# Kernel tuning notes

Measured on AMD Instinct MI355X. Metric: run time of the kernel, lower is better.

## Reference

```python
import jax, jax.numpy as jnp
import numpy as np
from jax import lax

KS = 3
N = KS * KS  # 9 sampling locations per output pixel


def conv2d(x, w, b, pad, dil=1):
    out = lax.conv_general_dilated(
        x, w, window_strides=(1, 1), padding=((pad, pad), (pad, pad)),
        rhs_dilation=(dil, dil), dimension_numbers=('NCHW', 'OIHW', 'NCHW'))
    return out + b[None, :, None, None]


def deform_conv(x, p_w, p_b, dw, db):
    # Pure deform-conv-v2 semantics: offsets from p_conv, bilinear gather on
    # zero-padded input, then 3x3 contraction over the 9 gathered samples.
    B, C, H, W = x.shape
    offset = conv2d(x, p_w, p_b, 1)                       # (B, 2N, H, W)
    xp = jnp.pad(x, ((0, 0), (0, 0), (1, 1), (1, 1)))     # zero pad by 1
    Hp, Wp = H + 2, W + 2
    rr = jnp.arange(-(KS // 2), KS // 2 + 1)
    pi, pj = jnp.meshgrid(rr, rr, indexing='ij')
    p_n = jnp.concatenate([pi.reshape(-1), pj.reshape(-1)]).astype(x.dtype)   # (2N,)
    gi, gj = jnp.meshgrid(jnp.arange(1, H + 1), jnp.arange(1, W + 1), indexing='ij')
    p0 = jnp.concatenate([jnp.broadcast_to(gi, (N, H, W)),
                          jnp.broadcast_to(gj, (N, H, W))], 0).astype(x.dtype)  # (2N,H,W)
    p = p0[None] + p_n[None, :, None, None] + offset      # (B, 2N, H, W)
    p = jnp.transpose(p, (0, 2, 3, 1))                    # (B, H, W, 2N)
    py, px = p[..., :N], p[..., N:]
    fy, fx = jnp.floor(py), jnp.floor(px)
    lt_y = jnp.clip(fy, 0, Hp - 1); lt_x = jnp.clip(fx, 0, Wp - 1)
    rb_y = jnp.clip(fy + 1, 0, Hp - 1); rb_x = jnp.clip(fx + 1, 0, Wp - 1)
    pyc = jnp.clip(py, 0, Hp - 1); pxc = jnp.clip(px, 0, Wp - 1)
    g_lt = (1 + (lt_y - pyc)) * (1 + (lt_x - pxc))
    g_rb = (1 - (rb_y - pyc)) * (1 - (rb_x - pxc))
    g_lb = (1 + (lt_y - pyc)) * (1 - (rb_x - pxc))
    g_rt = (1 - (rb_y - pyc)) * (1 + (lt_x - pxc))
    xf = xp.reshape(B, C, Hp * Wp)

    def gather(qy, qx):
        idx = (qy.astype(jnp.int32) * Wp + qx.astype(jnp.int32)).reshape(B, -1)
        g = jax.vmap(lambda xb, ib: jnp.take(xb, ib, axis=1))(xf, idx)
        return g.reshape(B, C, H, W, N)

    x_lt = gather(lt_y, lt_x); x_rb = gather(rb_y, rb_x)
    x_lb = gather(lt_y, rb_x); x_rt = gather(rb_y, lt_x)
    samples = (g_lt[:, None] * x_lt + g_rb[:, None] * x_rb
               + g_lb[:, None] * x_lb + g_rt[:, None] * x_rt)  # (B,C,H,W,N)
    out = jnp.einsum('bchwn,ocn->bohw', samples, dw.reshape(dw.shape[0], C, N))
    return out + db[None, :, None, None]


def reference(x, w1, b1, w2, b2, w3, b3, w4, b4, p_w, p_b, dw, db, cw, cb):
    branches = [(w1, b1, 1, 1.0), (w2, b2, 3, 3.0), (w3, b3, 5, 5.0), (w4, b4, 7, 7.0)]
    feats = [deform_conv(conv2d(x, w, b, d, d) * s, p_w, p_b, dw, db)
             for (w, b, d, s) in branches]
    combined = jnp.concatenate(feats, axis=1)             # (B, 4*Cout, H, W)
    return jax.nn.relu(conv2d(combined, cw, cb, 0))


def setup_inputs() -> dict:
    B, Cin, Cout, H, W = 4, 128, 64, 128, 128
    key = jax.random.key(0)
    ks = jax.random.split(key, 16)
    sc3 = 1.0 / np.sqrt(Cin * 9)      # fan-in scale for 3x3 convs
    sc1 = 1.0 / np.sqrt(4 * Cout)     # fan-in scale for 1x1 fuse conv
    scd = 1.0 / np.sqrt(Cout * 9)     # deform main conv
    inp = {'x': jax.random.normal(ks[0], (B, Cin, H, W), jnp.float32)}
    for i in range(4):
        inp[f'w{i+1}'] = jax.random.normal(ks[1 + i], (Cout, Cin, 3, 3), jnp.float32) * sc3
        inp[f'b{i+1}'] = jax.random.normal(ks[5 + i], (Cout,), jnp.float32) * 0.01
    inp['p_w'] = jax.random.normal(ks[9], (2 * N, Cout, 3, 3), jnp.float32) * 0.01
    inp['p_b'] = jax.random.normal(ks[10], (2 * N,), jnp.float32) * 0.01
    inp['dw'] = jax.random.normal(ks[11], (Cout, Cout, 3, 3), jnp.float32) * scd
    inp['db'] = jax.random.normal(ks[12], (Cout,), jnp.float32) * 0.01
    inp['cw'] = jax.random.normal(ks[13], (Cout, 4 * Cout, 1, 1), jnp.float32) * sc1
    inp['cb'] = jax.random.normal(ks[14], (Cout,), jnp.float32) * 0.01
    return inp
```

## Files before the change

kernel.cpp:

```cpp
#include <hip/hip_runtime.h>
#include <hip/hip_fp16.h>

#define H 128
#define W 128
#define CIN 128
#define COUT 64
#define HW (H*W)
#define XW 130
#define FSL (XW*XW*64)
#define XTD 144

typedef __half f16;
typedef __attribute__((ext_vector_type(8)))  _Float16 h16x8;
typedef __attribute__((ext_vector_type(16))) float f32x16;

__device__ __forceinline__ float b2f(f16 v){ return __half2float(v); }
__device__ __forceinline__ f16  f2b(float v){ return __float2half_rn(v); }
__device__ __forceinline__ unsigned pack2(float a, float b){
    unsigned short ua = __builtin_bit_cast(unsigned short, f2b(a));
    unsigned short ub = __builtin_bit_cast(unsigned short, f2b(b));
    return (unsigned)ua | ((unsigned)ub << 16);
}
__device__ __forceinline__ unsigned short b16u(float v){
    return __builtin_bit_cast(unsigned short, f2b(v));
}
__device__ __forceinline__ __half2 uh2(unsigned u){
    return __builtin_bit_cast(__half2, u);
}
__device__ __forceinline__ unsigned h2u(__half2 v){
    return __builtin_bit_cast(unsigned, v);
}
__device__ __forceinline__ unsigned bcasth2(float v){
    __half h = __float2half_rn(v);
    return h2u(__halves2half2(h, h));
}
__device__ __forceinline__ void gld16(const void* g, void* l){
    __builtin_amdgcn_global_load_lds(
        (const __attribute__((address_space(1))) void*)g,
        (__attribute__((address_space(3))) void*)l, 16, 0, 0);
}

__global__ __launch_bounds__(256) void k_prep(
    const float* __restrict__ w1, const float* __restrict__ w2,
    const float* __restrict__ w3, const float* __restrict__ w4,
    const float* __restrict__ dw, const float* __restrict__ cw,
    const float* __restrict__ pw,
    uint4* __restrict__ xt4, unsigned* __restrict__ wbt,
    unsigned* __restrict__ dwb2, unsigned* __restrict__ cwb2,
    unsigned* __restrict__ pwb)
{
    int bid = blockIdx.x;
    int t = threadIdx.x;
    if (bid < 1024){
        const int n4 = (4*XTD*XTD*64)/4;
        for (int i = bid*256 + t; i < n4; i += 1024*256)
            xt4[i] = make_uint4(0,0,0,0);
    } else if (bid < 1600){
        int tid = (bid-1024)*256 + t;
        int cpl = tid & 7;
        int oc  = (tid >> 3) & 63;
        int tap = (tid >> 9) % 9;
        int cg  = (tid / 4608) & 7;
        int d   = tid / 36864;
        const float* wt = (d==0)?w1:(d==1)?w2:(d==2)?w3:w4;
        int c = cg*8 + cpl;
        wbt[tid] = pack2(wt[((size_t)oc*CIN + 2*c  )*9 + tap],
                         wt[((size_t)oc*CIN + 2*c+1)*9 + tap]);
    } else if (bid < 1672){
        int i = (bid-1600)*256 + t;
        int n = i>>11;
        int s = (i>>9)&3;
        int hf = (i>>8)&1;
        int oc = (i>>2)&63;
        int cl = i&3;
        int cp = s*8 + hf*4 + cl;
        dwb2[i] = pack2(dw[((size_t)oc*64 + 2*cp  )*9 + n],
                        dw[((size_t)oc*64 + 2*cp+1)*9 + n]);
    } else if (bid < 1704){
        int i = (bid-1672)*256 + t;
        int kc = i>>9;
        int hf = (i>>8)&1;
        int oc = (i>>2)&63;
        int cl = i&3;
        int cp = kc*8 + hf*4 + cl;
        cwb2[i] = pack2(cw[(size_t)oc*256 + 2*cp], cw[(size_t)oc*256 + 2*cp+1]);
    } else {
        int i = (bid-1704)*256 + t;
        int cl = i & 3, oc = (i>>2)&31, hf = (i>>7)&1, cq = (i>>8)&3, tap = i>>10;
        int c = cq*16 + hf*8 + cl*2;
        unsigned v = 0u;
        if (oc < 18)
            v = pack2(pw[((size_t)oc*64 + c  )*9 + tap],
                      pw[((size_t)oc*64 + c+1)*9 + tap]);
        pwb[i] = v;
    }
}

__global__ __launch_bounds__(256) void k_xprep(
    const float* __restrict__ x, unsigned* __restrict__ xt)
{
    int y = blockIdx.x, b = blockIdx.y;
    int t = threadIdx.x;
    __shared__ float xsm[64*131];
    for (int ci0 = 0; ci0 < 128; ci0 += 64){
        for (int i=0;i<32;i++){
            int idx = t + 256*i;
            int col = idx & 127, ci = idx >> 7;
            xsm[ci*131 + col] = x[(((size_t)b*CIN + ci0+ci)*H + y)*W + col];
        }
        __syncthreads();
        for (int i=0;i<16;i++){
            int idx = t + 256*i;
            int cpg = idx & 31, col = idx >> 5;
            int cgg = (ci0 >> 4) + (cpg >> 3);
            int cpl = cpg & 7;
            unsigned u = pack2(xsm[(2*cpg)*131 + col], xsm[(2*cpg+1)*131 + col]);
            xt[((((size_t)b*8 + cgg)*XTD + y+8)*XTD + col+8)*8 + cpl] = u;
        }
        __syncthreads();
    }
}

__global__ __launch_bounds__(256,3) void k_branch_mfma(
    const unsigned* __restrict__ xt, const unsigned* __restrict__ wbt,
    const float* __restrict__ b1, const float* __restrict__ b2,
    const float* __restrict__ b3, const float* __restrict__ b4,
    f16* __restrict__ feats2)
{
    int bid = blockIdx.x;
    int xcd = bid & 7;
    int j   = bid >> 3;
    int zb  = xcd + 8*(j & 1);
    int hp  = j >> 1;
    int d = zb >> 2, b = zb & 3;
    int dil = 2*d + 1;
    int h0 = hp*2;
    const float* bs = (d==0)?b1:(d==1)?b2:(d==2)?b3:b4;
    const float scale = (float)dil;

    __shared__ unsigned smem[6912 + 4608];
    unsigned* As = smem;
    unsigned* Bs = smem + 6912;
    const unsigned short* As16 = (const unsigned short*)As;
    const unsigned short* Bs16 = (const unsigned short*)Bs;

    int t = threadIdx.x;
    int lane = t & 63;
    int w = t >> 6;
    int l31 = lane & 31;
    int half = lane >> 5;

    f16* fb = feats2 + (size_t)zb*FSL;
    if (t < 32){
        int yy = h0 + 1 + (t>>4);
        int side = (t>>3)&1;
        int q = t & 7;
        uint4 z = make_uint4(0,0,0,0);
        *(uint4*)((unsigned short*)fb + ((size_t)yy*XW + side*129)*64 + q*8) = z;
    }
    if (hp == 0){
        uint4 z = make_uint4(0,0,0,0);
        for (int i=t; i<2080; i+=256){
            int row = i / 1040;
            int r = i % 1040;
            int xx = r >> 3, q = r & 7;
            *(uint4*)((unsigned short*)fb + ((size_t)(row*129)*XW + xx)*64 + q*8) = z;
        }
    }

    f32x16 acc[2][2];
    #pragma unroll
    for (int i=0;i<2;i++)
      #pragma unroll
      for (int jj=0;jj<2;jj++)
        #pragma unroll
        for (int e=0;e<16;e++) acc[i][jj][e] = 0.f;

    const unsigned* xtb_b = xt + (size_t)b*8*XTD*XTD*8;
    int r = w >> 1;
    int pxb = (w & 1) * 64;

    for (int cg=0; cg<8; cg++){
        const unsigned* xs_cg = xtb_b + (size_t)cg*XTD*XTD*8;
        #pragma unroll
        for (int i=0;i<7;i++){
            int idx4 = t + 256*i;
            if (idx4 < 1728){
                int row6 = idx4 / 288;
                int rem  = idx4 - row6*288;
                int hf   = rem / 144;
                int s    = rem - hf*144;
                int ky = row6 >> 1, rr = row6 & 1;
                int yy = h0 + rr + (ky-1)*dil + 8;
                gld16(xs_cg + ((size_t)yy*XTD + (s + 8 - dil))*8 + hf*4,
                      &As[idx4*4]);
            }
        }
        const unsigned* wb_cg = wbt + ((size_t)d*8 + cg)*4608;
        #pragma unroll
        for (int i=0;i<5;i++){
            int idx4 = t + 256*i;
            if (idx4 < 1152){
                int tap = idx4 >> 7;
                int hf  = (idx4 >> 6) & 1;
                int oc  = idx4 & 63;
                gld16(wb_cg + ((size_t)tap*64 + oc)*8 + hf*4,
                      &Bs[idx4*4]);
            }
        }
        __syncthreads();
        #pragma unroll
        for (int tap=0; tap<9; tap++){
            int ky = tap/3, kx = tap%3;
            int arow = ((ky*2 + r)*2 + half)*144;
            int brow = (tap*2 + half)*64;
            h16x8 a0  = *(const h16x8*)(As16 + (arow + pxb      + l31 + kx*dil)*8);
            h16x8 a1  = *(const h16x8*)(As16 + (arow + pxb + 32 + l31 + kx*dil)*8);
            h16x8 bb0 = *(const h16x8*)(Bs16 + (brow      + l31)*8);
            h16x8 bb1 = *(const h16x8*)(Bs16 + (brow + 32 + l31)*8);
            acc[0][0] = __builtin_amdgcn_mfma_f32_32x32x16_f16(a0, bb0, acc[0][0], 0,0,0);
            acc[0][1] = __builtin_amdgcn_mfma_f32_32x32x16_f16(a0, bb1, acc[0][1], 0,0,0);
            acc[1][0] = __builtin_amdgcn_mfma_f32_32x32x16_f16(a1, bb0, acc[1][0], 0,0,0);
            acc[1][1] = __builtin_amdgcn_mfma_f32_32x32x16_f16(a1, bb1, acc[1][1], 0,0,0);
        }
        __syncthreads();
    }

    unsigned short* ep = (unsigned short*)smem;
    float bias0 = bs[l31], bias1 = bs[32 + l31];
    #pragma unroll
    for (int i=0;i<2;i++){
      #pragma unroll
      for (int jj=0;jj<2;jj++){
        int oc = jj*32 + l31;
        float bj = jj ? bias1 : bias0;
        #pragma unroll
        for (int rg=0; rg<4; rg++){
            int m0 = 64*w + 32*i + 8*rg + 4*half;
            #pragma unroll
            for (int e=0;e<4;e++)
                ep[(m0+e)*64 + oc] = b16u((acc[i][jj][4*rg+e] + bj)*scale);
        }
      }
    }
    __syncthreads();
    {
        int row = t >> 7, pxm = t & 127;
        unsigned short* drow = (unsigned short*)fb + ((size_t)(h0+1+row)*XW + pxm + 1)*64;
        const unsigned short* srow = ep + t*64;
        #pragma unroll
        for (int q=0;q<8;q++)
            *(uint4*)(drow + q*8) = *(const uint4*)(srow + q*8);
    }
}

__global__ __launch_bounds__(256,2) void k_offset_mfma(
    const f16* __restrict__ feats2,
    const unsigned* __restrict__ pwb,
    const float* __restrict__ pb,
    f16* __restrict__ offs)
{
    int bid = blockIdx.x;
    int xcd  = bid & 7;
    int h    = (bid >> 3) & 127;
    int pass = bid >> 10;
    int zb   = xcd + 8*pass;

    int t = threadIdx.x;
    int lane = t & 63, w = t >> 6;
    int l31 = lane & 31, half = lane >> 5;

    __shared__ unsigned short xs[3*132*68];

    const unsigned short* fin = (const unsigned short*)(feats2 + (size_t)zb*FSL);
    for (int i=t; i<3120; i+=256){
        int row = i / 1040;
        int r   = i % 1040;
        int col = r >> 3, q = r & 7;
        uint4 v = *(const uint4*)(fin + ((size_t)(h+row)*XW + col)*64 + q*8);
        *(uint4*)&xs[(row*132 + col)*68 + q*8] = v;
    }
    __syncthreads();

    f32x16 acc;
    #pragma unroll
    for (int e=0;e<16;e++) acc[e] = 0.f;

    int pxw = 32*w + l31;
    #pragma unroll
    for (int tap=0; tap<9; tap++){
        int ky = tap/3, kx = tap%3;
        const unsigned short* arow = &xs[(ky*132 + pxw + kx)*68 + half*8];
        const unsigned* brow = pwb + (((size_t)tap*4)*2 + half)*128 + l31*4;
        #pragma unroll
        for (int cq=0; cq<4; cq++){
            h16x8 a  = *(const h16x8*)(arow + cq*16);
            h16x8 b0 = *(const h16x8*)(brow + cq*256);
            acc = __builtin_amdgcn_mfma_f32_32x32x16_f16(a, b0, acc, 0,0,0);
        }
    }
    __syncthreads();

    unsigned short* ep = (unsigned short*)xs;
    if (l31 < 18){
        float bias = pb[l31];
        #pragma unroll
        for (int rg=0; rg<4; rg++){
            int m0 = 32*w + 4*half + 8*rg;
            #pragma unroll
            for (int e=0;e<4;e++)
                ep[l31*132 + m0+e] = b16u(acc[4*rg+e] + bias);
        }
    }
    __syncthreads();
    unsigned short* obase = (unsigned short*)(offs + (size_t)zb*18*HW) ;
    for (int i=t; i<288; i+=256){
        int oc = i >> 4, sg = i & 15;
        *(uint4*)(obase + (size_t)oc*HW + h*W + sg*8) = *(const uint4*)(ep + oc*132 + sg*8);
    }
}

__device__ __forceinline__ void coords_px(
    const f16* __restrict__ obase, int h, int n, int px, unsigned* cp)
{
    float offy = b2f(obase[n*HW + px]);
    float offx = b2f(obase[(n+9)*HW + px]);
    float py  = (float)(h + n/3) + offy;
    float pxf = (float)(px + n%3) + offx;
    float fy = floorf(py), fx = floorf(pxf);
    float lty = fminf(fmaxf(fy,     0.f),129.f);
    float ltx = fminf(fmaxf(fx,     0.f),129.f);
    float rby = fminf(fmaxf(fy+1.f, 0.f),129.f);
    float rbx = fminf(fmaxf(fx+1.f, 0.f),129.f);
    float pyc = fminf(fmaxf(py,     0.f),129.f);
    float pxc = fminf(fmaxf(pxf,    0.f),129.f);
    float ay = 1.f + (lty-pyc), by = 1.f - (rby-pyc);
    float ax = 1.f + (ltx-pxc), bx = 1.f - (rbx-pxc);
    cp[0] = bcasth2(ay*ax);
    cp[1] = bcasth2(ay*bx);
    cp[2] = bcasth2(by*ax);
    cp[3] = bcasth2(by*bx);
    cp[4] = (unsigned)(((int)lty*XW + (int)ltx)*64);
    cp[5] = (unsigned)(((int)rbx - (int)ltx)*64);
    cp[6] = (unsigned)(((int)rby - (int)lty)*XW*64);
}

__global__ __launch_bounds__(256,6) void k_deform_mfma(
    const f16* __restrict__ feats2,
    const f16* __restrict__ offs,
    const unsigned* __restrict__ dwb2,
    const float* __restrict__ db,
    f16* __restrict__ dout2)
{
    int bid = blockIdx.x;
    int xcd  = bid & 7;
    int h    = (bid >> 3) & 127;
    int pass = bid >> 10;
    int zb   = xcd + 8*pass;

    int t = threadIdx.x;
    int lane = t & 63, w = t >> 6;
    int l31 = lane & 31, half = lane >> 5;
    int pxg = t >> 3;
    int cq  = t & 7;
    int sub_w = cq >> 1;
    int hf8   = cq & 1;

    #define AROW 516
    __shared__ unsigned smem_d[8*AROW + 2048];
    unsigned* Asu = smem_d;
    unsigned* Cd  = smem_d + 8*AROW;

    const f16* obase = offs + (size_t)zb*18*HW + h*W;
    const unsigned short* fbase = (const unsigned short*)(feats2 + (size_t)zb*FSL);

    f32x16 acc0, acc1;
    #pragma unroll
    for (int e=0;e<16;e++){ acc0[e]=0.f; acc1[e]=0.f; }

    if (t < 128) coords_px(obase, h, 0, t, Cd + t*8);
    __syncthreads();

    for (int n=0; n<9; n++){
        unsigned* Cdc = Cd + (n&1)*1024;
        unsigned* Cdn = Cd + ((n+1)&1)*1024;

        #pragma unroll
        for (int s=0; s<4; s++){
            int px = s*32 + pxg;
            const unsigned* cp = Cdc + px*8;
            uint4 c0 = *(const uint4*)cp;
            uint4 c1 = *(const uint4*)(cp + 4);
            __half2 wlt = uh2(c0.x);
            __half2 wlb = uh2(c0.y);
            __half2 wrt = uh2(c0.z);
            __half2 wrb = uh2(c0.w);
            int dxo = (int)c1.y, dyo = (int)c1.z;
            const unsigned short* fc = fbase + (int)c1.x + cq*8;
            unsigned LT[4], LB[4], RT[4], RB[4];
            *(uint4*)LT = *(const uint4*)(fc);
            *(uint4*)LB = *(const uint4*)(fc+dxo);
            *(uint4*)RT = *(const uint4*)(fc+dyo);
            *(uint4*)RB = *(const uint4*)(fc+dyo+dxo);
            unsigned pk[4];
            #pragma unroll
            for (int jq=0;jq<4;jq++){
                __half2 r = __hmul2(wlt, uh2(LT[jq]));
                r = __hfma2(wlb, uh2(LB[jq]), r);
                r = __hfma2(wrt, uh2(RT[jq]), r);
                r = __hfma2(wrb, uh2(RB[jq]), r);
                pk[jq] = h2u(r);
            }
            uint4 av; av.x=pk[0]; av.y=pk[1]; av.z=pk[2]; av.w=pk[3];
            *(uint4*)&Asu[(sub_w*2 + hf8)*AROW + px*4] = av;
        }
        if (n < 8 && t < 128) coords_px(obase, h, n+1, t, Cdn + t*8);
        __syncthreads();

        const unsigned short* As16 = (const unsigned short*)Asu;
        const unsigned short* dnb16 = (const unsigned short*)(dwb2 + n*2048);
        #pragma unroll
        for (int s=0;s<4;s++){
            h16x8 a  = *(const h16x8*)(As16 + (s*2+half)*(AROW*2) + (32*w + l31)*8);
            h16x8 b0 = *(const h16x8*)(dnb16 + ((s*2+half)*64 + l31)*8);
            h16x8 b1 = *(const h16x8*)(dnb16 + ((s*2+half)*64 + 32+l31)*8);
            acc0 = __builtin_amdgcn_mfma_f32_32x32x16_f16(a, b0, acc0, 0,0,0);
            acc1 = __builtin_amdgcn_mfma_f32_32x32x16_f16(a, b1, acc1, 0,0,0);
        }
        __syncthreads();
    }

    unsigned short* ep = (unsigned short*)smem_d;
    #pragma unroll
    for (int nt=0; nt<2; nt++){
        int oc = nt*32 + l31;
        float bias = db[oc];
        const f32x16& A = nt ? acc1 : acc0;
        #pragma unroll
        for (int rg=0; rg<4; rg++){
            int m0 = 32*w + 4*half + 8*rg;
            #pragma unroll
            for (int e=0;e<4;e++)
                ep[(m0+e)*64 + oc] = b16u(A[4*rg+e] + bias);
        }
    }
    __syncthreads();
    uint4* dst = (uint4*)((unsigned short*)dout2 + ((size_t)zb*128 + h)*(128*64));
    #pragma unroll
    for (int i=0;i<4;i++)
        dst[t + 256*i] = ((const uint4*)ep)[t + 256*i];
    #undef AROW
}

__global__ __launch_bounds__(256,2) void k_combine_mfma(
    const f16* __restrict__ dout2,
    const unsigned* __restrict__ cwb2,
    const float* __restrict__ cb,
    float* __restrict__ out)
{
    int h = blockIdx.x, b = blockIdx.y;
    int t = threadIdx.x;
    int lane = t & 63, w = t >> 6, l31 = lane & 31, half = lane >> 5;

    __shared__ float ep2[64*132];

    f32x16 acc0, acc1;
    #pragma unroll
    for (int e=0;e<16;e++){ acc0[e]=0.f; acc1[e]=0.f; }

    const unsigned short* dbase0 = (const unsigned short*)dout2;
    const unsigned short* cb16 = (const unsigned short*)cwb2;
    size_t rowsel2 = ((size_t)b*128 + h)*128 + (32*w + l31);

    unsigned AV[64];
    #pragma unroll
    for (int kc=0; kc<16; kc++){
        *(uint4*)&AV[kc*4] = *(const uint4*)(
            dbase0 + (size_t)(kc>>2)*(4*HW*64) + rowsel2*64 + (kc&3)*16 + half*8);
    }
    #pragma unroll
    for (int kc=0; kc<16; kc++){
        h16x8 a  = __builtin_bit_cast(h16x8, *(uint4*)&AV[kc*4]);
        h16x8 b0 = *(const h16x8*)(cb16 + ((kc*2+half)*64 + l31)*8);
        h16x8 b1 = *(const h16x8*)(cb16 + ((kc*2+half)*64 + 32+l31)*8);
        acc0 = __builtin_amdgcn_mfma_f32_32x32x16_f16(a, b0, acc0, 0,0,0);
        acc1 = __builtin_amdgcn_mfma_f32_32x32x16_f16(a, b1, acc1, 0,0,0);
    }

    #pragma unroll
    for (int nt=0; nt<2; nt++){
        int oc = nt*32 + l31;
        float bias = cb[oc];
        const f32x16& A = nt ? acc1 : acc0;
        #pragma unroll
        for (int rg=0; rg<4; rg++){
            int m0 = 32*w + 4*half + 8*rg;
            #pragma unroll
            for (int e=0;e<4;e++)
                ep2[oc*132 + m0+e] = fmaxf(A[4*rg+e] + bias, 0.f);
        }
    }
    __syncthreads();
    for (int i=t; i<2048; i+=256){
        int oc = i>>5, sg = i&31;
        *(uint4*)&out[(((size_t)b*64+oc)*128 + h)*128 + sg*4] = *(const uint4*)&ep2[oc*132 + sg*4];
    }
}

extern "C" void kernel_launch(void* const* d_in, const int* in_sizes, int n_in,
                              void* d_out, int out_size, void* d_ws, size_t ws_size,
                              hipStream_t stream) {
    const float* x  = (const float*)d_in[0];
    const float* w1 = (const float*)d_in[1];
    const float* b1 = (const float*)d_in[2];
    const float* w2 = (const float*)d_in[3];
    const float* b2 = (const float*)d_in[4];
    const float* w3 = (const float*)d_in[5];
    const float* b3 = (const float*)d_in[6];
    const float* w4 = (const float*)d_in[7];
    const float* b4 = (const float*)d_in[8];
    const float* pw = (const float*)d_in[9];
    const float* pb = (const float*)d_in[10];
    const float* dw = (const float*)d_in[11];
    const float* db = (const float*)d_in[12];
    const float* cw = (const float*)d_in[13];
    const float* cb = (const float*)d_in[14];
    float* out = (float*)d_out;

    f16* feats2 = (f16*)d_ws;
    f16* offs   = feats2 + (size_t)16*FSL;
    f16* region2 = offs + (size_t)16*18*HW;
    f16* dout2  = region2;
    unsigned* xt  = (unsigned*)region2;
    unsigned* wbt = xt + (size_t)4*8*XTD*XTD*8;
    unsigned* dwb2 = (unsigned*)(dout2 + (size_t)16*128*128*64);
    unsigned* cwb2 = dwb2 + 18432;
    unsigned* pwb  = cwb2 + 8192;

    k_prep        <<<dim3(1740),    256, 0, stream>>>(w1,w2,w3,w4, dw, cw, pw,
                                                      (uint4*)xt, wbt, dwb2, cwb2, pwb);
    k_xprep       <<<dim3(128,4),   256, 0, stream>>>(x, xt);
    k_branch_mfma <<<dim3(1024),    256, 0, stream>>>(xt, wbt, b1,b2,b3,b4, feats2);
    k_offset_mfma <<<dim3(2048),    256, 0, stream>>>(feats2, pwb, pb, offs);
    k_deform_mfma <<<dim3(2048),    256, 0, stream>>>(feats2, offs, dwb2, db, dout2);
    k_combine_mfma<<<dim3(128,4),   256, 0, stream>>>(dout2, cwb2, cb, out);
}
```

Baseline: 301.2 us.

## Stage deform weights in LDS and software-pipeline bilinear gathers in deform kernel

The per-tap deform weight slice is now copied into a padded LDS buffer, with a new oc-major packing layout, instead of each wave reading B fragments from global memory. The gather loop is unrolled into two interleaved register sets so the four corner loads of the next pixel group are in flight while the current one is interpolated. The coordinate computation is no longer double-buffered one tap ahead; it is done inline at the top of each tap, which adds a sync-separated serial step. More registers and LDS per block, so launch bounds drop occupancy from 6 to 4 blocks per CU.

```diff
diff --git a/kernel.cpp b/kernel.cpp
--- a/kernel.cpp
+++ b/kernel.cpp
@@ -68,12 +68,7 @@
                          wt[((size_t)oc*CIN + 2*c+1)*9 + tap]);
     } else if (bid < 1672){
         int i = (bid-1600)*256 + t;
-        int n = i>>11;
-        int s = (i>>9)&3;
-        int hf = (i>>8)&1;
-        int oc = (i>>2)&63;
-        int cl = i&3;
-        int cp = s*8 + hf*4 + cl;
+        int n = i>>11, oc = (i>>5)&63, cp = i&31;
         dwb2[i] = pack2(dw[((size_t)oc*64 + 2*cp  )*9 + n],
                         dw[((size_t)oc*64 + 2*cp+1)*9 + n]);
     } else if (bid < 1704){
@@ -320,32 +315,7 @@
     }
 }
 
-__device__ __forceinline__ void coords_px(
-    const f16* __restrict__ obase, int h, int n, int px, unsigned* cp)
-{
-    float offy = b2f(obase[n*HW + px]);
-    float offx = b2f(obase[(n+9)*HW + px]);
-    float py  = (float)(h + n/3) + offy;
-    float pxf = (float)(px + n%3) + offx;
-    float fy = floorf(py), fx = floorf(pxf);
-    float lty = fminf(fmaxf(fy,     0.f),129.f);
-    float ltx = fminf(fmaxf(fx,     0.f),129.f);
-    float rby = fminf(fmaxf(fy+1.f, 0.f),129.f);
-    float rbx = fminf(fmaxf(fx+1.f, 0.f),129.f);
-    float pyc = fminf(fmaxf(py,     0.f),129.f);
-    float pxc = fminf(fmaxf(pxf,    0.f),129.f);
-    float ay = 1.f + (lty-pyc), by = 1.f - (rby-pyc);
-    float ax = 1.f + (ltx-pxc), bx = 1.f - (rbx-pxc);
-    cp[0] = bcasth2(ay*ax);
-    cp[1] = bcasth2(ay*bx);
-    cp[2] = bcasth2(by*ax);
-    cp[3] = bcasth2(by*bx);
-    cp[4] = (unsigned)(((int)lty*XW + (int)ltx)*64);
-    cp[5] = (unsigned)(((int)rbx - (int)ltx)*64);
-    cp[6] = (unsigned)(((int)rby - (int)lty)*XW*64);
-}
-
-__global__ __launch_bounds__(256,6) void k_deform_mfma(
+__global__ __launch_bounds__(256,4) void k_deform_mfma(
     const f16* __restrict__ feats2,
     const f16* __restrict__ offs,
     const unsigned* __restrict__ dwb2,
@@ -367,9 +337,10 @@
     int hf8   = cq & 1;
 
     #define AROW 516
-    __shared__ unsigned smem_d[8*AROW + 2048];
+    __shared__ unsigned smem_d[8*AROW + 2304 + 1024];
     unsigned* Asu = smem_d;
-    unsigned* Cd  = smem_d + 8*AROW;
+    unsigned* Bsu = smem_d + 8*AROW;
+    unsigned* Cd  = smem_d + 8*AROW + 2304;
 
     const f16* obase = offs + (size_t)zb*18*HW + h*W;
     const unsigned short* fbase = (const unsigned short*)(feats2 + (size_t)zb*FSL);
@@ -378,57 +349,96 @@
     #pragma unroll
     for (int e=0;e<16;e++){ acc0[e]=0.f; acc1[e]=0.f; }
 
-    if (t < 128) coords_px(obase, h, 0, t, Cd + t*8);
-    __syncthreads();
+#define CLOAD(S, C0, C1) { \
+    const unsigned* cp_ = Cd + ((S)*32 + pxg)*8; \
+    C0 = *(const uint4*)cp_; \
+    C1 = *(const uint4*)(cp_ + 4); }
+#define GLOAD(C1, LT, LB, RT, RB) { \
+    int dxo_ = (int)(C1).y, dyo_ = (int)(C1).z; \
+    const unsigned short* fc_ = fbase + (int)(C1).x + cq*8; \
+    LT = *(const uint4*)(fc_); \
+    LB = *(const uint4*)(fc_ + dxo_); \
+    RT = *(const uint4*)(fc_ + dyo_); \
+    RB = *(const uint4*)(fc_ + dyo_ + dxo_); }
+#define INTERP(S, C0, LT, LB, RT, RB) { \
+    __half2 wlt_ = uh2((C0).x), wlb_ = uh2((C0).y); \
+    __half2 wrt_ = uh2((C0).z), wrb_ = uh2((C0).w); \
+    unsigned p0_,p1_,p2_,p3_; \
+    { __half2 r_ = __hmul2(wlt_, uh2((LT).x)); r_ = __hfma2(wlb_, uh2((LB).x), r_); \
+      r_ = __hfma2(wrt_, uh2((RT).x), r_); r_ = __hfma2(wrb_, uh2((RB).x), r_); p0_ = h2u(r_); } \
+    { __half2 r_ = __hmul2(wlt_, uh2((LT).y)); r_ = __hfma2(wlb_, uh2((LB).y), r_); \
+      r_ = __hfma2(wrt_, uh2((RT).y), r_); r_ = __hfma2(wrb_, uh2((RB).y), r_); p1_ = h2u(r_); } \
+    { __half2 r_ = __hmul2(wlt_, uh2((LT).z)); r_ = __hfma2(wlb_, uh2((LB).z), r_); \
+      r_ = __hfma2(wrt_, uh2((RT).z), r_); r_ = __hfma2(wrb_, uh2((RB).z), r_); p2_ = h2u(r_); } \
+    { __half2 r_ = __hmul2(wlt_, uh2((LT).w)); r_ = __hfma2(wlb_, uh2((LB).w), r_); \
+      r_ = __hfma2(wrt_, uh2((RT).w), r_); r_ = __hfma2(wrb_, uh2((RB).w), r_); p3_ = h2u(r_); } \
+    uint4 av_; av_.x=p0_; av_.y=p1_; av_.z=p2_; av_.w=p3_; \
+    *(uint4*)&Asu[(sub_w*2 + hf8)*AROW + ((S)*32 + pxg)*4] = av_; }
 
     for (int n=0; n<9; n++){
-        unsigned* Cdc = Cd + (n&1)*1024;
-        unsigned* Cdn = Cd + ((n+1)&1)*1024;
-
-        #pragma unroll
-        for (int s=0; s<4; s++){
-            int px = s*32 + pxg;
-            const unsigned* cp = Cdc + px*8;
-            uint4 c0 = *(const uint4*)cp;
-            uint4 c1 = *(const uint4*)(cp + 4);
-            __half2 wlt = uh2(c0.x);
-            __half2 wlb = uh2(c0.y);
-            __half2 wrt = uh2(c0.z);
-            __half2 wrb = uh2(c0.w);
-            int dxo = (int)c1.y, dyo = (int)c1.z;
-            const unsigned short* fc = fbase + (int)c1.x + cq*8;
-            unsigned LT[4], LB[4], RT[4], RB[4];
-            *(uint4*)LT = *(const uint4*)(fc);
-            *(uint4*)LB = *(const uint4*)(fc+dxo);
-            *(uint4*)RT = *(const uint4*)(fc+dyo);
-            *(uint4*)RB = *(const uint4*)(fc+dyo+dxo);
-            unsigned pk[4];
-            #pragma unroll
-            for (int jq=0;jq<4;jq++){
-                __half2 r = __hmul2(wlt, uh2(LT[jq]));
-                r = __hfma2(wlb, uh2(LB[jq]), r);
-                r = __hfma2(wrt, uh2(RT[jq]), r);
-                r = __hfma2(wrb, uh2(RB[jq]), r);
-                pk[jq] = h2u(r);
-            }
-            uint4 av; av.x=pk[0]; av.y=pk[1]; av.z=pk[2]; av.w=pk[3];
-            *(uint4*)&Asu[(sub_w*2 + hf8)*AROW + px*4] = av;
-        }
-        if (n < 8 && t < 128) coords_px(obase, h, n+1, t, Cdn + t*8);
+        const uint4* dsrc = (const uint4*)(dwb2 + n*2048);
+        #pragma unroll
+        for (int i=0;i<2;i++){
+            int j = t + 256*i;
+            int idx4 = j*4;
+            int oc = idx4 >> 5, cp = idx4 & 31;
+            *(uint4*)&Bsu[oc*36 + cp] = dsrc[j];
+        }
+        if (t < 128){
+            float offy = b2f(obase[n*HW + t]);
+            float offx = b2f(obase[(n+9)*HW + t]);
+            float py  = (float)(h + n/3) + offy;
+            float pxf = (float)(t + n%3) + offx;
+            float fy = floorf(py), fx = floorf(pxf);
+            float lty = fminf(fmaxf(fy,     0.f),129.f);
+            float ltx = fminf(fmaxf(fx,     0.f),129.f);
+            float rby = fminf(fmaxf(fy+1.f, 0.f),129.f);
+            float rbx = fminf(fmaxf(fx+1.f, 0.f),129.f);
+            float pyc = fminf(fmaxf(py,     0.f),129.f);
+            float pxc = fminf(fmaxf(pxf,    0.f),129.f);
+            float ay = 1.f + (lty-pyc), by = 1.f - (rby-pyc);
+            float ax = 1.f + (ltx-pxc), bx = 1.f - (rbx-pxc);
+            unsigned* cp = &Cd[t*8];
+            cp[0] = bcasth2(ay*ax);
+            cp[1] = bcasth2(ay*bx);
+            cp[2] = bcasth2(by*ax);
+            cp[3] = bcasth2(by*bx);
+            cp[4] = (unsigned)(((int)lty*XW + (int)ltx)*64);
+            cp[5] = (unsigned)(((int)rbx - (int)ltx)*64);
+            cp[6] = (unsigned)(((int)rby - (int)lty)*XW*64);
+        }
+        __syncthreads();
+
+        {
+            uint4 c0a, c1a, c0b, c1b;
+            uint4 LTa, LBa, RTa, RBa;
+            uint4 LTb, LBb, RTb, RBb;
+            CLOAD(0, c0a, c1a); GLOAD(c1a, LTa, LBa, RTa, RBa);
+            CLOAD(1, c0b, c1b); GLOAD(c1b, LTb, LBb, RTb, RBb);
+            INTERP(0, c0a, LTa, LBa, RTa, RBa);
+            CLOAD(2, c0a, c1a); GLOAD(c1a, LTa, LBa, RTa, RBa);
+            INTERP(1, c0b, LTb, LBb, RTb, RBb);
+            CLOAD(3, c0b, c1b); GLOAD(c1b, LTb, LBb, RTb, RBb);
+            INTERP(2, c0a, LTa, LBa, RTa, RBa);
+            INTERP(3, c0b, LTb, LBb, RTb, RBb);
+        }
         __syncthreads();
 
         const unsigned short* As16 = (const unsigned short*)Asu;
-        const unsigned short* dnb16 = (const unsigned short*)(dwb2 + n*2048);
+        const unsigned short* Bs16 = (const unsigned short*)Bsu;
         #pragma unroll
         for (int s=0;s<4;s++){
             h16x8 a  = *(const h16x8*)(As16 + (s*2+half)*(AROW*2) + (32*w + l31)*8);
-            h16x8 b0 = *(const h16x8*)(dnb16 + ((s*2+half)*64 + l31)*8);
-            h16x8 b1 = *(const h16x8*)(dnb16 + ((s*2+half)*64 + 32+l31)*8);
+            h16x8 b0 = *(const h16x8*)(Bs16 + (l31*36 + s*8 + half*4)*2);
+            h16x8 b1 = *(const h16x8*)(Bs16 + ((32+l31)*36 + s*8 + half*4)*2);
             acc0 = __builtin_amdgcn_mfma_f32_32x32x16_f16(a, b0, acc0, 0,0,0);
             acc1 = __builtin_amdgcn_mfma_f32_32x32x16_f16(a, b1, acc1, 0,0,0);
         }
         __syncthreads();
     }
+#undef CLOAD
+#undef GLOAD
+#undef INTERP
 
     unsigned short* ep = (unsigned short*)smem_d;
     #pragma unroll
```

New measurement: 291.8 us. 3.1% less time.
